# Optimization experiments

Measured on AMD Instinct MI355X. Metric: run time of the kernel, lower is better.

## Reference

```python
import jax, jax.numpy as jnp
import numpy as np

H_, W_, KNN, KO = 64, 64, 32, 32
TAU, ETA, LAMBDA0, ALPHA = 1.5, 8.0, 0.001, 10.0
A_, B_, BETA, BETA_P = 1.0, 0.0, 8.0, 8.0
SMOOTH_KS, SMOOTH_SIGMA, EPS = 5, 1.0, 1e-6


def _base_grid(h, w):
    ys = jnp.arange(h, dtype=jnp.float32)
    xs = jnp.arange(w, dtype=jnp.float32)
    yy, xx = jnp.meshgrid(ys, xs, indexing='ij')
    return jnp.stack([xx.reshape(-1), yy.reshape(-1)], axis=-1)  # (N,2) as (x,y)


def _offset_bins(K_o, h, w):
    maxr = (h ** 2 + w ** 2) ** 0.5 * 0.5
    ks = jnp.arange(1, K_o + 1, dtype=jnp.float32)
    angles = 2.0 * jnp.pi * (ks - 1) / K_o
    radii = 0.2 * maxr + 0.6 * maxr * (ks - 1) / (K_o - 1 + 1e-9)
    return jnp.stack([radii * jnp.cos(angles), radii * jnp.sin(angles)], axis=-1)  # (K_o,2)


def _gaussian_kernel(ks, sigma):
    ax = jnp.arange(-(ks // 2), ks // 2 + 1, dtype=jnp.float32)  # matches torch -ks//2+1 .. ks//2 for odd ks
    xx, yy = jnp.meshgrid(ax, ax, indexing='ij')
    k = jnp.exp(-(xx ** 2 + yy ** 2) / (2.0 * sigma ** 2))
    return (k / k.sum()).reshape(1, 1, ks, ks)


def setup_inputs() -> dict:
    key = jax.random.key(0)
    k1, k2 = jax.random.split(key)
    B, N = 2, H_ * W_
    E = jax.random.normal(k1, (B, N, 256), dtype=jnp.float32)
    A0 = jax.random.uniform(k2, (B, N, N), dtype=jnp.float32)
    return {
        'E': E,
        'A0': A0,
        'P': _base_grid(H_, W_),
        'bins': _offset_bins(KO, H_, W_),
        'smooth_kernel': _gaussian_kernel(SMOOTH_KS, SMOOTH_SIGMA),
    }


def reference(E, A0, P, bins, smooth_kernel):
    B, N, _ = A0.shape
    # top-k neighbors per row (sorted descending, like torch.topk)
    topk_vals, topk_idx = jax.lax.top_k(A0, KNN)  # (B,N,k)

    # offset vectors to neighbors
    p_j = P[topk_idx]                              # (B,N,k,2)
    v = p_j - P[None, :, None, :]                  # (B,N,k,2)
    diff = v[..., None, :] - bins[None, None, None, :, :]   # (B,N,k,K_o,2)
    dist2 = (diff ** 2).sum(-1)                    # (B,N,k,K_o)
    kappa = jnp.exp(-dist2 / (2.0 * TAU ** 2 + 1e-12))

    # global bin histogram and softmax weights
    Hbins = (topk_vals[..., None] * kappa).sum(axis=(1, 2))   # (B,K_o)
    Wsoft = jax.nn.softmax(ETA * Hbins, axis=-1)              # (B,K_o)

    R_edges = LAMBDA0 + (Wsoft[:, None, None, :] * kappa).sum(-1)  # (B,N,k)
    tildeA = topk_vals * R_edges
    A1_edges = tildeA / (tildeA.sum(-1, keepdims=True) + EPS)

    # entropy -> backgroundness U
    p = jax.nn.softmax(ALPHA * A1_edges, axis=-1)
    entropy = -(p * jnp.log(p + EPS)).sum(-1)      # (B,N)
    U = jax.nn.sigmoid(-A_ * entropy + B_)
    m = 1.0 - U

    # mask both endpoints of each edge
    m_j = jax.vmap(jnp.take)(m, topk_idx)          # (B,N,k)
    hatA = m[:, :, None] * A1_edges * m_j
    A2_edges = hatA / (hatA.sum(-1, keepdims=True) + EPS)

    # scatter sparse edges back to dense NxN (row indices unique per row)
    b_idx = jnp.arange(B)[:, None, None]
    n_idx = jnp.arange(N)[None, :, None]
    A2_dense = jnp.zeros((B, N, N), A2_edges.dtype).at[b_idx, n_idx, topk_idx].set(A2_edges)
    A2_dense = A2_dense / (A2_dense.sum(-1, keepdims=True) + EPS)

    # directional evidence
    exp_fwd = jnp.exp(BETA * A2_dense)
    exp_rev = jnp.swapaxes(exp_fwd, -1, -2)
    P_dir = exp_fwd / (exp_fwd + exp_rev + EPS)
    eye = jnp.eye(N, dtype=A2_dense.dtype)
    P_dir = P_dir * (1.0 - eye)                    # zero diagonal
    s_ev = (A2_dense * P_dir).sum(-1)
    A2_T = jnp.swapaxes(A2_dense, -1, -2)
    t_ev = (A2_T * (1.0 - jnp.swapaxes(P_dir, -1, -2))).sum(-1)
    pi_src = s_ev / (s_ev + t_ev + EPS)
    pi_tgt = 1.0 - pi_src

    # spatial attention map
    W_mean = Wsoft.mean(0)                         # (K_o,)
    chi = (kappa * W_mean[None, None, None, :]).sum(-1)       # (B,N,k)
    w_local = jax.nn.softmax(BETA_P * A2_edges, axis=-1)
    q = (w_local * chi).sum(-1)                    # (B,N)
    A1_map = q.reshape(B, 1, H_, W_)
    pad = SMOOTH_KS // 2
    smoothed = jax.lax.conv_general_dilated(A1_map, smooth_kernel, (1, 1), [(pad, pad), (pad, pad)])
    A1_map = jax.nn.sigmoid(smoothed)              # (B,1,h,w)

    return (A2_dense, U, pi_src, pi_tgt, A1_map)
```

## Files before the change

### kernel.cpp

```cpp
#include <hip/hip_runtime.h>
#include <math.h>

#define NN 4096
#define KK 32
#define KOb 32
#define BB 2
#define NSLOT 64

constexpr float EPS = 1e-6f;

#define WS_VALS   0
#define WS_IDX    (WS_VALS + BB*NN*KK)
#define WS_HBP    (WS_IDX + BB*NN*KK)
#define WS_A1     (WS_HBP + BB*NSLOT*KOb)
#define WS_M      (WS_A1 + BB*NN*KK)
#define WS_CHI    (WS_M + BB*NN)
#define WS_A2     (WS_CHI + BB*NN*KK)
#define WS_SEV    (WS_A2 + BB*NN*KK)
#define WS_TEV    (WS_SEV + BB*NN)
#define WS_Q      (WS_TEV + BB*NN)

#define OUT_A2   0
#define OUT_U    ((size_t)BB*NN*NN)
#define OUT_PSRC (OUT_U + BB*NN)
#define OUT_PTGT (OUT_PSRC + BB*NN)
#define OUT_MAP  (OUT_PTGT + BB*NN)

__device__ __forceinline__ unsigned int fkey(float x) {
    unsigned int u = __float_as_uint(x);
    return u ^ ((unsigned int)((int)u >> 31) | 0x80000000u);
}
__device__ __forceinline__ float key2f(unsigned int k) {
    unsigned int u = (k & 0x80000000u) ? (k ^ 0x80000000u) : ~k;
    return __uint_as_float(u);
}

__global__ __launch_bounds__(256) void k_topk(const float* __restrict__ A0,
                                              const float* __restrict__ bins,
                                              float* __restrict__ ws) {
    __shared__ float sbins[2 * KOb];
    __shared__ int   scnt[4];
    __shared__ int   swtot[4];
    __shared__ unsigned long long cand[64];
    __shared__ float selv[KK], seldx[KK], seldy[KK];
    __shared__ float shb[KOb];

    const int t = threadIdx.x;
    const int wv = t >> 6, lane = t & 63;
    const int R = blockIdx.x;
    const int b = R >> 12;
    const int r = R & (NN - 1);

    if (t < 2 * KOb) sbins[t] = bins[t];
    if (t < KOb) shb[t] = 0.f;

    const float4* row4 = (const float4*)(A0 + (size_t)R * NN);
    unsigned int key[16];
    #pragma unroll
    for (int i = 0; i < 4; ++i) {
        const float4 f = row4[i * 256 + t];
        key[4 * i + 0] = fkey(f.x);
        key[4 * i + 1] = fkey(f.y);
        key[4 * i + 2] = fkey(f.z);
        key[4 * i + 3] = fkey(f.w);
    }

    unsigned int lo = 0u, hi = 0xFFFFFFFFu;
    int cnt = NN, it = 0;
    while (cnt > 64) {
        unsigned int mid;
        if (it == 0)      mid = 0xBF7E0000u;
        else if (it == 1) mid = 0xBF7C4000u;
        else              mid = lo + ((hi - lo) >> 1);
        if (mid <= lo || mid >= hi) mid = lo + ((hi - lo) >> 1);
        if (mid == lo) break;
        int cl = 0;
        #pragma unroll
        for (int j = 0; j < 16; ++j) cl += (key[j] > mid) ? 1 : 0;
        int c = cl;
        #pragma unroll
        for (int m = 32; m >= 1; m >>= 1) c += __shfl_xor(c, m);
        if (lane == 0) scnt[wv] = c;
        __syncthreads();
        const int ctot = scnt[0] + scnt[1] + scnt[2] + scnt[3];
        __syncthreads();
        if (ctot >= KK) { lo = mid; cnt = ctot; } else hi = mid;
        if (++it > 48) break;
    }

    int cl = 0;
    #pragma unroll
    for (int j = 0; j < 16; ++j) cl += (key[j] > lo) ? 1 : 0;
    int inc = cl;
    #pragma unroll
    for (int m = 1; m < 64; m <<= 1) {
        const int o = __shfl_up(inc, m);
        if (lane >= m) inc += o;
    }
    if (lane == 63) swtot[wv] = inc;
    __syncthreads();
    int off = inc - cl;
    #pragma unroll
    for (int w = 0; w < 4; ++w) if (w < wv) off += swtot[w];
    const int nc0 = swtot[0] + swtot[1] + swtot[2] + swtot[3];
    const int ncand = (nc0 < 64) ? nc0 : 64;

    int slot = off;
    #pragma unroll
    for (int j = 0; j < 16; ++j) {
        if (key[j] > lo && slot < 64) {
            const unsigned int gidx = (unsigned int)((j >> 2) * 1024 + t * 4 + (j & 3));
            cand[slot] = ((unsigned long long)key[j] << 32)
                       | (unsigned long long)(4095u - gidx);
            ++slot;
        }
    }
    __syncthreads();

    if (t < 64) {
        const unsigned long long cd = (t < ncand) ? cand[t] : 0ull;
        int rank = 0;
        #pragma unroll
        for (int i = 0; i < 64; ++i) {
            const unsigned long long o = __shfl(cd, i);
            rank += (o > cd) ? 1 : 0;
        }
        if (t < ncand && rank < KK) {
            const float val = key2f((unsigned int)(cd >> 32));
            const int gidx = 4095 - (int)(cd & 0xFFFull);
            ws[WS_VALS + (size_t)R * KK + rank] = val;
            ((int*)(ws + WS_IDX))[(size_t)R * KK + rank] = gidx;
            selv[rank]  = val;
            seldx[rank] = (float)((gidx & 63) - (r & 63));
            seldy[rank] = (float)((gidx >> 6) - (r >> 6));
        }
    }
    __syncthreads();

    const int e = t >> 3;
    const float v = selv[e], dx0 = seldx[e], dy0 = seldy[e];
    #pragma unroll
    for (int jj = 0; jj < 4; ++jj) {
        const int o = (lane & 7) * 4 + jj;
        const float dx = dx0 - sbins[2 * o], dy = dy0 - sbins[2 * o + 1];
        float contrib = v * __expf(-(dx * dx + dy * dy) * (1.0f / 4.5f));
        contrib += __shfl_xor(contrib, 8);
        contrib += __shfl_xor(contrib, 16);
        contrib += __shfl_xor(contrib, 32);
        if ((lane >> 3) == 0) atomicAdd(&shb[o], contrib);
    }
    __syncthreads();
    if (t < KOb)
        atomicAdd(ws + WS_HBP + b * (NSLOT * KOb) + (R & (NSLOT - 1)) * KOb + t,
                  shb[t]);
}

__global__ __launch_bounds__(256) void k_row1(const float* __restrict__ bins,
                                              float* __restrict__ ws,
                                              float* __restrict__ out_u) {
    __shared__ float sbins[2 * KOb], sHB[BB * KOb], swsoft[BB * KOb], swmean[KOb];
    const int t = threadIdx.x;
    if (t < 2 * KOb) sbins[t] = bins[t];
    if (t >= 64 && t < 64 + BB * KOb) sHB[t - 64] = 0.f;
    __syncthreads();

    #pragma unroll
    for (int rep = 0; rep < 2; ++rep) {
        const int task = t + 256 * rep;
        const int bo = task & 63;
        const int sg = task >> 6;
        float ps = 0.f;
        #pragma unroll
        for (int s = 0; s < 8; ++s)
            ps += ws[WS_HBP + (bo >> 5) * (NSLOT * KOb) + (sg * 8 + s) * KOb + (bo & 31)];
        atomicAdd(&sHB[bo], ps);
    }
    __syncthreads();
    if (t < BB * KOb) {
        const float h = 8.0f * sHB[t];
        float mx = h;
        #pragma unroll
        for (int m = 16; m >= 1; m >>= 1) mx = fmaxf(mx, __shfl_xor(mx, m));
        const float e = __expf(h - mx);
        float s = e;
        #pragma unroll
        for (int m = 16; m >= 1; m >>= 1) s += __shfl_xor(s, m);
        swsoft[t] = e / s;
    }
    if (t < KOb) swmean[t] = 0.5f * (swsoft[t] + swsoft[KOb + t]);
    __syncthreads();

    const int wv = t >> 6, lane = t & 63;
    const int R = blockIdx.x * 4 + wv;
    const int b = R >> 12;
    const int r = R & (NN - 1);
    const bool act = lane < 32;
    const int k = lane;

    float val = 0.f, Redge = 0.f, chi = 0.f;
    if (act) {
        val = ws[WS_VALS + (size_t)R * KK + k];
        const int c = ((int*)(ws + WS_IDX))[(size_t)R * KK + k];
        const float dx0 = (float)((c & 63) - (r & 63));
        const float dy0 = (float)((c >> 6) - (r >> 6));
        float racc = 0.f, cacc = 0.f;
        for (int o = 0; o < KOb; ++o) {
            const float dx = dx0 - sbins[2 * o], dy = dy0 - sbins[2 * o + 1];
            const float kap = __expf(-(dx * dx + dy * dy) * (1.0f / 4.5f));
            racc += swsoft[b * KOb + o] * kap;
            cacc += swmean[o] * kap;
        }
        Redge = 0.001f + racc;
        chi = cacc;
    }
    const float tilde = act ? val * Redge : 0.f;
    float s = tilde;
    #pragma unroll
    for (int m = 16; m >= 1; m >>= 1) s += __shfl_xor(s, m);
    const float a1 = tilde / (s + EPS);

    const float z = act ? 10.f * a1 : -1e30f;
    float mz = z;
    #pragma unroll
    for (int m = 16; m >= 1; m >>= 1) mz = fmaxf(mz, __shfl_xor(mz, m));
    const float e = act ? __expf(z - mz) : 0.f;
    float se = e;
    #pragma unroll
    for (int m = 16; m >= 1; m >>= 1) se += __shfl_xor(se, m);
    const float p = e / se;
    const float ent_t = act ? -p * __logf(p + EPS) : 0.f;
    float ent = ent_t;
    #pragma unroll
    for (int m = 16; m >= 1; m >>= 1) ent += __shfl_xor(ent, m);
    const float U = 1.f / (1.f + __expf(ent));

    if (act) {
        ws[WS_A1  + (size_t)R * KK + k] = a1;
        ws[WS_CHI + (size_t)R * KK + k] = chi;
    }
    if (lane == 0) { out_u[R] = U; ws[WS_M + R] = 1.f - U; }
}

__global__ __launch_bounds__(256) void k_row2d(float* __restrict__ ws,
                                               float* __restrict__ outA2) {
    __shared__ float srow[NN];
    __shared__ float sdv[KK];
    __shared__ int   sidx[KK];
    const int R = blockIdx.x;
    const int b = R >> 12;
    const int r = R & (NN - 1);
    const int t = threadIdx.x;

    const int gid = blockIdx.x * 256 + t;
    if (gid < BB * NN) ws[WS_TEV + gid] = 0.f;

    float4* s4 = (float4*)srow;
    const float4 z4 = make_float4(0.f, 0.f, 0.f, 0.f);
    #pragma unroll
    for (int i = 0; i < 4; ++i) s4[t + 256 * i] = z4;

    if (t < 64) {
        const int lane = t;
        const bool act = lane < 32;
        const int k = lane;
        const float mi = ws[WS_M + R];
        float a1 = 0.f; int c = 0; float mj = 0.f;
        if (act) {
            a1 = ws[WS_A1 + (size_t)R * KK + k];
            c = ((int*)(ws + WS_IDX))[(size_t)R * KK + k];
            mj = ws[WS_M + b * NN + c];
        }
        const float hat = act ? mi * a1 * mj : 0.f;
        float S = hat;
        #pragma unroll
        for (int m = 16; m >= 1; m >>= 1) S += __shfl_xor(S, m);
        const float a2e = hat / (S + EPS);
        float S2 = a2e;
        #pragma unroll
        for (int m = 16; m >= 1; m >>= 1) S2 += __shfl_xor(S2, m);
        const float dv = a2e / (S2 + EPS);

        const float z = act ? 8.f * a2e : -1e30f;
        float mz = z;
        #pragma unroll
        for (int m = 16; m >= 1; m >>= 1) mz = fmaxf(mz, __shfl_xor(mz, m));
        const float e = act ? __expf(z - mz) : 0.f;
        float se = e;
        #pragma unroll
        for (int m = 16; m >= 1; m >>= 1) se += __shfl_xor(se, m);
        const float wl = e / se;
        const float chi = act ? ws[WS_CHI + (size_t)R * KK + k] : 0.f;
        float q = act ? wl * chi : 0.f;
        #pragma unroll
        for (int m = 16; m >= 1; m >>= 1) q += __shfl_xor(q, m);
        if (lane == 0) ws[WS_Q + R] = q;

        if (act) {
            ws[WS_A2 + (size_t)R * KK + k] = dv;
            sdv[k] = dv;
            sidx[k] = c;
        }
    }
    __syncthreads();
    if (t < KK) srow[sidx[t]] = sdv[t];
    __syncthreads();
    float4* o4 = (float4*)(outA2 + (size_t)b * NN * NN + (size_t)r * NN);
    #pragma unroll
    for (int i = 0; i < 4; ++i) o4[t + 256 * i] = s4[t + 256 * i];
}

__global__ __launch_bounds__(256) void k_dir(float* __restrict__ ws) {
    const int t = threadIdx.x;
    const int wv = t >> 6, lane = t & 63;
    const int R = blockIdx.x * 4 + wv;
    const int b = R >> 12;
    const int r = R & (NN - 1);
    const bool act = lane < 32;
    const int k = lane;

    float a = 0.f; int c = r;
    if (act) {
        a = ws[WS_A2 + (size_t)R * KK + k];
        c = ((int*)(ws + WS_IDX))[(size_t)R * KK + k];
    }
    float pdir = 0.f;
    if (act && c != r) {
        const int4* irow = (const int4*)((const int*)(ws + WS_IDX)
                                         + (size_t)(b * NN + c) * KK);
        int p = -1;
        #pragma unroll
        for (int q = 0; q < 8; ++q) {
            const int4 i4 = irow[q];
            if (i4.x == r) p = q * 4 + 0;
            if (i4.y == r) p = q * 4 + 1;
            if (i4.z == r) p = q * 4 + 2;
            if (i4.w == r) p = q * 4 + 3;
        }
        const float arev = (p >= 0) ? ws[WS_A2 + (size_t)(b * NN + c) * KK + p] : 0.f;
        const float ef = __expf(8.f * a), er = __expf(8.f * arev);
        pdir = ef / (ef + er + EPS);
    }
    float s = a * pdir;
    #pragma unroll
    for (int m = 16; m >= 1; m >>= 1) s += __shfl_xor(s, m);
    if (lane == 0) ws[WS_SEV + R] = s;
    if (act) atomicAdd(ws + WS_TEV + b * NN + c, a * (1.f - pdir));
}

__global__ void k_tail(const float* __restrict__ ws, const float* __restrict__ kern,
                       float* __restrict__ out_psrc, float* __restrict__ out_ptgt,
                       float* __restrict__ out_map) {
    const int i = blockIdx.x * 256 + threadIdx.x;
    const float s = ws[WS_SEV + i], tv = ws[WS_TEV + i];
    const float ps = s / (s + tv + EPS);
    out_psrc[i] = ps;
    out_ptgt[i] = 1.f - ps;

    const int b = i >> 12;
    const int pix = i & 4095;
    const int y = pix >> 6, x = pix & 63;
    float acc = 0.f;
    #pragma unroll
    for (int ky = 0; ky < 5; ++ky) {
        const int yy = y + ky - 2;
        if (yy < 0 || yy >= 64) continue;
        #pragma unroll
        for (int kx = 0; kx < 5; ++kx) {
            const int xx = x + kx - 2;
            if (xx < 0 || xx >= 64) continue;
            acc += ws[WS_Q + b * 4096 + yy * 64 + xx] * kern[ky * 5 + kx];
        }
    }
    out_map[i] = 1.f / (1.f + __expf(-acc));
}

extern "C" void kernel_launch(void* const* d_in, const int* in_sizes, int n_in,
                              void* d_out, int out_size, void* d_ws, size_t ws_size,
                              hipStream_t stream) {
    const float* A0   = (const float*)d_in[1];
    const float* bins = (const float*)d_in[3];
    const float* kern = (const float*)d_in[4];
    float* out = (float*)d_out;
    float* ws  = (float*)d_ws;

    hipMemsetAsync(ws + WS_HBP, 0, BB * NSLOT * KOb * sizeof(float), stream);

    k_topk <<<BB * NN,       256, 0, stream>>>(A0, bins, ws);
    k_row1 <<<BB * NN / 4,   256, 0, stream>>>(bins, ws, out + OUT_U);
    k_row2d<<<BB * NN,       256, 0, stream>>>(ws, out);
    k_dir  <<<BB * NN / 4,   256, 0, stream>>>(ws);
    k_tail <<<BB * NN / 256, 256, 0, stream>>>(ws, kern,
                                               out + OUT_PSRC, out + OUT_PTGT,
                                               out + OUT_MAP);
}
```

Baseline: 296.8 us.

## Fuse all stages into one cooperative kernel with grid-wide syncs

Replaces the five-kernel pipeline (topk, row1, row2d, dir, tail) with a single cooperative kernel of 512 blocks. Each block processes 16 rows through every stage, separated by grid.sync(). The histogram is reduced into a global buffer, and the zeroing of that buffer and of the t-evidence accumulator moves into one widened memset. The aim is to remove launch gaps and intermediate kernel boundaries. The cost is far fewer resident blocks while streaming A0 reads and dense A2 writes, plus serialized per-row dense writes inside each block. A fallback to the old kernels runs if the occupancy check or the cooperative launch fails.

Result: slower. 592.3 us (+99.6%).

```diff
diff --git a/kernel.cpp b/kernel.cpp
--- a/kernel.cpp
+++ b/kernel.cpp
@@ -1,24 +1,31 @@
 #include <hip/hip_runtime.h>
+#include <hip/hip_cooperative_groups.h>
 #include <math.h>
+
+namespace cg = cooperative_groups;
 
 #define NN 4096
 #define KK 32
 #define KOb 32
 #define BB 2
 #define NSLOT 64
+#define NB 512
+#define RPB (BB*NN/NB)
 
 constexpr float EPS = 1e-6f;
 
-#define WS_VALS   0
-#define WS_IDX    (WS_VALS + BB*NN*KK)
-#define WS_HBP    (WS_IDX + BB*NN*KK)
-#define WS_A1     (WS_HBP + BB*NSLOT*KOb)
-#define WS_M      (WS_A1 + BB*NN*KK)
-#define WS_CHI    (WS_M + BB*NN)
-#define WS_A2     (WS_CHI + BB*NN*KK)
-#define WS_SEV    (WS_A2 + BB*NN*KK)
-#define WS_TEV    (WS_SEV + BB*NN)
-#define WS_Q      (WS_TEV + BB*NN)
+#define WS_VALS  0
+#define WS_IDX   (WS_VALS + BB*NN*KK)
+#define WS_A1    (WS_IDX + BB*NN*KK)
+#define WS_CHI   (WS_A1 + BB*NN*KK)
+#define WS_A2    (WS_CHI + BB*NN*KK)
+#define WS_M     (WS_A2 + BB*NN*KK)
+#define WS_SEV   (WS_M + BB*NN)
+#define WS_Q     (WS_SEV + BB*NN)
+#define WS_HBP   (WS_Q + BB*NN)
+#define WS_HB    (WS_HBP + BB*NSLOT*KOb)
+#define WS_TEV   (WS_HB + BB*KOb)
+#define WS_ZSPAN (BB*NSLOT*KOb + BB*KOb + BB*NN)
 
 #define OUT_A2   0
 #define OUT_U    ((size_t)BB*NN*NN)
@@ -33,6 +40,329 @@
 __device__ __forceinline__ float key2f(unsigned int k) {
     unsigned int u = (k & 0x80000000u) ? (k ^ 0x80000000u) : ~k;
     return __uint_as_float(u);
+}
+
+__global__ __launch_bounds__(256, 4) void kfused(const float* __restrict__ A0,
+                                                 const float* __restrict__ bins,
+                                                 const float* __restrict__ kern,
+                                                 float* __restrict__ ws,
+                                                 float* __restrict__ out) {
+    cg::grid_group grid = cg::this_grid();
+
+    __shared__ float sbins[2 * KOb];
+    __shared__ float shb[KOb];
+    __shared__ int   scnt[4], swtot[4];
+    __shared__ unsigned long long cand[64];
+    __shared__ float selv[KK], seldx[KK], seldy[KK];
+    __shared__ float swsoft[BB * KOb], swmean[KOb];
+    __shared__ float sdv[4][KK];
+    __shared__ int   sidx[4][KK];
+    __shared__ float srow[NN];
+
+    const int t = threadIdx.x;
+    const int wv = t >> 6, lane = t & 63;
+    const int bk = blockIdx.x;
+    const int b = bk >> 8;
+
+    if (t < 2 * KOb) sbins[t] = bins[t];
+    if (t < KOb) shb[t] = 0.f;
+    __syncthreads();
+
+    for (int rr = 0; rr < RPB; ++rr) {
+        const int R = bk * RPB + rr;
+        const int r = R & (NN - 1);
+
+        const float4* row4 = (const float4*)(A0 + (size_t)R * NN);
+        unsigned int key[16];
+        #pragma unroll
+        for (int i = 0; i < 4; ++i) {
+            const float4 f = row4[i * 256 + t];
+            key[4 * i + 0] = fkey(f.x);
+            key[4 * i + 1] = fkey(f.y);
+            key[4 * i + 2] = fkey(f.z);
+            key[4 * i + 3] = fkey(f.w);
+        }
+
+        unsigned int lo = 0u, hi = 0xFFFFFFFFu;
+        int cnt = NN, it = 0;
+        while (cnt > 64) {
+            unsigned int mid;
+            if (it == 0)      mid = 0xBF7E0000u;
+            else if (it == 1) mid = 0xBF7C4000u;
+            else              mid = lo + ((hi - lo) >> 1);
+            if (mid <= lo || mid >= hi) mid = lo + ((hi - lo) >> 1);
+            if (mid == lo) break;
+            int cl = 0;
+            #pragma unroll
+            for (int j = 0; j < 16; ++j) cl += (key[j] > mid) ? 1 : 0;
+            int c = cl;
+            #pragma unroll
+            for (int m = 32; m >= 1; m >>= 1) c += __shfl_xor(c, m);
+            if (lane == 0) scnt[wv] = c;
+            __syncthreads();
+            const int ctot = scnt[0] + scnt[1] + scnt[2] + scnt[3];
+            __syncthreads();
+            if (ctot >= KK) { lo = mid; cnt = ctot; } else hi = mid;
+            if (++it > 48) break;
+        }
+
+        int cl = 0;
+        #pragma unroll
+        for (int j = 0; j < 16; ++j) cl += (key[j] > lo) ? 1 : 0;
+        int inc = cl;
+        #pragma unroll
+        for (int m = 1; m < 64; m <<= 1) {
+            const int o = __shfl_up(inc, m);
+            if (lane >= m) inc += o;
+        }
+        if (lane == 63) swtot[wv] = inc;
+        __syncthreads();
+        int off = inc - cl;
+        #pragma unroll
+        for (int w = 0; w < 4; ++w) if (w < wv) off += swtot[w];
+        const int nc0 = swtot[0] + swtot[1] + swtot[2] + swtot[3];
+        const int ncand = (nc0 < 64) ? nc0 : 64;
+
+        int slot = off;
+        #pragma unroll
+        for (int j = 0; j < 16; ++j) {
+            if (key[j] > lo && slot < 64) {
+                const unsigned int gidx = (unsigned int)((j >> 2) * 1024 + t * 4 + (j & 3));
+                cand[slot] = ((unsigned long long)key[j] << 32)
+                           | (unsigned long long)(4095u - gidx);
+                ++slot;
+            }
+        }
+        __syncthreads();
+
+        if (t < 64) {
+            const unsigned long long cd = (t < ncand) ? cand[t] : 0ull;
+            int rank = 0;
+            #pragma unroll
+            for (int i = 0; i < 64; ++i) {
+                const unsigned long long o = __shfl(cd, i);
+                rank += (o > cd) ? 1 : 0;
+            }
+            if (t < ncand && rank < KK) {
+                const float val = key2f((unsigned int)(cd >> 32));
+                const int gidx = 4095 - (int)(cd & 0xFFFull);
+                ws[WS_VALS + (size_t)R * KK + rank] = val;
+                ((int*)(ws + WS_IDX))[(size_t)R * KK + rank] = gidx;
+                selv[rank]  = val;
+                seldx[rank] = (float)((gidx & 63) - (r & 63));
+                seldy[rank] = (float)((gidx >> 6) - (r >> 6));
+            }
+        }
+        __syncthreads();
+
+        const int e = t >> 3;
+        const float v = selv[e], dx0 = seldx[e], dy0 = seldy[e];
+        #pragma unroll
+        for (int jj = 0; jj < 4; ++jj) {
+            const int o = (lane & 7) * 4 + jj;
+            const float dx = dx0 - sbins[2 * o], dy = dy0 - sbins[2 * o + 1];
+            float contrib = v * __expf(-(dx * dx + dy * dy) * (1.0f / 4.5f));
+            contrib += __shfl_xor(contrib, 8);
+            contrib += __shfl_xor(contrib, 16);
+            contrib += __shfl_xor(contrib, 32);
+            if ((lane >> 3) == 0) atomicAdd(&shb[o], contrib);
+        }
+        __syncthreads();
+    }
+    if (t < KOb) atomicAdd(ws + WS_HB + b * KOb + t, shb[t]);
+
+    grid.sync();
+
+    if (t < BB * KOb) {
+        const float h = 8.0f * ws[WS_HB + t];
+        float mx = h;
+        #pragma unroll
+        for (int m = 16; m >= 1; m >>= 1) mx = fmaxf(mx, __shfl_xor(mx, m));
+        const float e = __expf(h - mx);
+        float s = e;
+        #pragma unroll
+        for (int m = 16; m >= 1; m >>= 1) s += __shfl_xor(s, m);
+        swsoft[t] = e / s;
+    }
+    __syncthreads();
+    if (t < KOb) swmean[t] = 0.5f * (swsoft[t] + swsoft[KOb + t]);
+    __syncthreads();
+
+    for (int it4 = 0; it4 < RPB / 4; ++it4) {
+        const int R = bk * RPB + it4 * 4 + wv;
+        const int r = R & (NN - 1);
+        const bool act = lane < 32;
+        const int k = lane;
+
+        float val = 0.f, Redge = 0.f, chi = 0.f;
+        if (act) {
+            val = ws[WS_VALS + (size_t)R * KK + k];
+            const int c = ((int*)(ws + WS_IDX))[(size_t)R * KK + k];
+            const float dx0 = (float)((c & 63) - (r & 63));
+            const float dy0 = (float)((c >> 6) - (r >> 6));
+            float racc = 0.f, cacc = 0.f;
+            for (int o = 0; o < KOb; ++o) {
+                const float dx = dx0 - sbins[2 * o], dy = dy0 - sbins[2 * o + 1];
+                const float kap = __expf(-(dx * dx + dy * dy) * (1.0f / 4.5f));
+                racc += swsoft[b * KOb + o] * kap;
+                cacc += swmean[o] * kap;
+            }
+            Redge = 0.001f + racc;
+            chi = cacc;
+        }
+        const float tilde = act ? val * Redge : 0.f;
+        float s = tilde;
+        #pragma unroll
+        for (int m = 16; m >= 1; m >>= 1) s += __shfl_xor(s, m);
+        const float a1 = tilde / (s + EPS);
+
+        const float z = act ? 10.f * a1 : -1e30f;
+        float mz = z;
+        #pragma unroll
+        for (int m = 16; m >= 1; m >>= 1) mz = fmaxf(mz, __shfl_xor(mz, m));
+        const float e = act ? __expf(z - mz) : 0.f;
+        float se = e;
+        #pragma unroll
+        for (int m = 16; m >= 1; m >>= 1) se += __shfl_xor(se, m);
+        const float p = e / se;
+        const float ent_t = act ? -p * __logf(p + EPS) : 0.f;
+        float ent = ent_t;
+        #pragma unroll
+        for (int m = 16; m >= 1; m >>= 1) ent += __shfl_xor(ent, m);
+        const float U = 1.f / (1.f + __expf(ent));
+
+        if (act) {
+            ws[WS_A1  + (size_t)R * KK + k] = a1;
+            ws[WS_CHI + (size_t)R * KK + k] = chi;
+        }
+        if (lane == 0) { out[OUT_U + R] = U; ws[WS_M + R] = 1.f - U; }
+    }
+
+    grid.sync();
+
+    for (int it4 = 0; it4 < RPB / 4; ++it4) {
+        const int R = bk * RPB + it4 * 4 + wv;
+        {
+            const bool act = lane < 32;
+            const int k = lane;
+            const float mi = ws[WS_M + R];
+            float a1 = 0.f; int c = 0; float mj = 0.f;
+            if (act) {
+                a1 = ws[WS_A1 + (size_t)R * KK + k];
+                c = ((int*)(ws + WS_IDX))[(size_t)R * KK + k];
+                mj = ws[WS_M + b * NN + c];
+            }
+            const float hat = act ? mi * a1 * mj : 0.f;
+            float S = hat;
+            #pragma unroll
+            for (int m = 16; m >= 1; m >>= 1) S += __shfl_xor(S, m);
+            const float a2e = hat / (S + EPS);
+            float S2 = a2e;
+            #pragma unroll
+            for (int m = 16; m >= 1; m >>= 1) S2 += __shfl_xor(S2, m);
+            const float dv = a2e / (S2 + EPS);
+
+            const float z = act ? 8.f * a2e : -1e30f;
+            float mz = z;
+            #pragma unroll
+            for (int m = 16; m >= 1; m >>= 1) mz = fmaxf(mz, __shfl_xor(mz, m));
+            const float e = act ? __expf(z - mz) : 0.f;
+            float se = e;
+            #pragma unroll
+            for (int m = 16; m >= 1; m >>= 1) se += __shfl_xor(se, m);
+            const float wl = e / se;
+            const float chi = act ? ws[WS_CHI + (size_t)R * KK + k] : 0.f;
+            float q = act ? wl * chi : 0.f;
+            #pragma unroll
+            for (int m = 16; m >= 1; m >>= 1) q += __shfl_xor(q, m);
+            if (lane == 0) ws[WS_Q + R] = q;
+
+            if (act) {
+                ws[WS_A2 + (size_t)R * KK + k] = dv;
+                sdv[wv][k] = dv;
+                sidx[wv][k] = c;
+            }
+        }
+        __syncthreads();
+        for (int sub = 0; sub < 4; ++sub) {
+            const int Rd = bk * RPB + it4 * 4 + sub;
+            float4* s4 = (float4*)srow;
+            const float4 z4 = make_float4(0.f, 0.f, 0.f, 0.f);
+            #pragma unroll
+            for (int i = 0; i < 4; ++i) s4[t + 256 * i] = z4;
+            __syncthreads();
+            if (t < KK) srow[sidx[sub][t]] = sdv[sub][t];
+            __syncthreads();
+            float4* o4 = (float4*)(out + (size_t)Rd * NN);
+            #pragma unroll
+            for (int i = 0; i < 4; ++i) o4[t + 256 * i] = s4[t + 256 * i];
+            __syncthreads();
+        }
+    }
+
+    grid.sync();
+
+    for (int it4 = 0; it4 < RPB / 4; ++it4) {
+        const int R = bk * RPB + it4 * 4 + wv;
+        const int r = R & (NN - 1);
+        const bool act = lane < 32;
+        const int k = lane;
+
+        float a = 0.f; int c = r;
+        if (act) {
+            a = ws[WS_A2 + (size_t)R * KK + k];
+            c = ((int*)(ws + WS_IDX))[(size_t)R * KK + k];
+        }
+        float pdir = 0.f;
+        if (act && c != r) {
+            const int4* irow = (const int4*)((const int*)(ws + WS_IDX)
+                                             + (size_t)(b * NN + c) * KK);
+            int p = -1;
+            #pragma unroll
+            for (int q = 0; q < 8; ++q) {
+                const int4 i4 = irow[q];
+                if (i4.x == r) p = q * 4 + 0;
+                if (i4.y == r) p = q * 4 + 1;
+                if (i4.z == r) p = q * 4 + 2;
+                if (i4.w == r) p = q * 4 + 3;
+            }
+            const float arev = (p >= 0) ? ws[WS_A2 + (size_t)(b * NN + c) * KK + p] : 0.f;
+            const float ef = __expf(8.f * a), er = __expf(8.f * arev);
+            pdir = ef / (ef + er + EPS);
+        }
+        float s = a * pdir;
+        #pragma unroll
+        for (int m = 16; m >= 1; m >>= 1) s += __shfl_xor(s, m);
+        if (lane == 0) ws[WS_SEV + R] = s;
+        if (act) atomicAdd(ws + WS_TEV + b * NN + c, a * (1.f - pdir));
+    }
+
+    grid.sync();
+
+    if (t < RPB) {
+        const int i = bk * RPB + t;
+        const float s = ws[WS_SEV + i], tv = ws[WS_TEV + i];
+        const float ps = s / (s + tv + EPS);
+        out[OUT_PSRC + i] = ps;
+        out[OUT_PTGT + i] = 1.f - ps;
+
+        const int bb = i >> 12;
+        const int pix = i & 4095;
+        const int y = pix >> 6, x = pix & 63;
+        float acc = 0.f;
+        #pragma unroll
+        for (int ky = 0; ky < 5; ++ky) {
+            const int yy = y + ky - 2;
+            if (yy < 0 || yy >= 64) continue;
+            #pragma unroll
+            for (int kx = 0; kx < 5; ++kx) {
+                const int xx = x + kx - 2;
+                if (xx < 0 || xx >= 64) continue;
+                acc += ws[WS_Q + bb * 4096 + yy * 64 + xx] * kern[ky * 5 + kx];
+            }
+        }
+        out[OUT_MAP + i] = 1.f / (1.f + __expf(-acc));
+    }
 }
 
 __global__ __launch_bounds__(256) void k_topk(const float* __restrict__ A0,
@@ -250,9 +580,7 @@
     const int b = R >> 12;
     const int r = R & (NN - 1);
     const int t = threadIdx.x;
-
-    const int gid = blockIdx.x * 256 + t;
-    if (gid < BB * NN) ws[WS_TEV + gid] = 0.f;
+    (void)r;
 
     float4* s4 = (float4*)srow;
     const float4 z4 = make_float4(0.f, 0.f, 0.f, 0.f);
@@ -304,7 +632,7 @@
     __syncthreads();
     if (t < KK) srow[sidx[t]] = sdv[t];
     __syncthreads();
-    float4* o4 = (float4*)(outA2 + (size_t)b * NN * NN + (size_t)r * NN);
+    float4* o4 = (float4*)(outA2 + (size_t)b * NN * NN + (size_t)(R & (NN - 1)) * NN);
     #pragma unroll
     for (int i = 0; i < 4; ++i) o4[t + 256 * i] = s4[t + 256 * i];
 }
@@ -383,7 +711,19 @@
     float* out = (float*)d_out;
     float* ws  = (float*)d_ws;
 
-    hipMemsetAsync(ws + WS_HBP, 0, BB * NSLOT * KOb * sizeof(float), stream);
+    hipMemsetAsync(ws + WS_HBP, 0, WS_ZSPAN * sizeof(float), stream);
+
+    int maxb = 0;
+    hipError_t qerr = hipOccupancyMaxActiveBlocksPerMultiprocessor(
+        &maxb, (const void*)kfused, 256, 0);
+    bool coop_ok = (qerr == hipSuccess) && (maxb * 256  >= NB);
+
+    if (coop_ok) {
+        void* args[] = { (void*)&A0, (void*)&bins, (void*)&kern, (void*)&ws, (void*)&out };
+        hipError_t lerr = hipLaunchCooperativeKernel((void*)kfused, dim3(NB), dim3(256),
+                                                     args, 0, stream);
+        if (lerr == hipSuccess) return;
+    }
 
     k_topk <<<BB * NN,       256, 0, stream>>>(A0, bins, ws);
     k_row1 <<<BB * NN / 4,   256, 0, stream>>>(bins, ws, out + OUT_U);
```
